# Performance work log

Measured on AMD Instinct MI355X. Metric: run time of the kernel, lower is better.

Reference implementation:

```python
import jax, jax.numpy as jnp
import numpy as np
from jax import lax

B, T, C, H, HOR = 64, 2048, 64, 256, 96
BETA, THR = 0.9, 1.0


def setup_inputs() -> dict:
    key = jax.random.key(0)
    ks = jax.random.split(key, 10)
    s = lambda *sh: 1.0 / np.sqrt(sh[-1])
    return {
        "x": jax.random.normal(ks[0], (B, T, C), jnp.float32),
        "snn_w": jax.random.uniform(ks[1], (H, C), jnp.float32, -s(C), s(C)),
        "snn_b": jax.random.uniform(ks[2], (H,), jnp.float32, -s(C), s(C)),
        "gru_wih": jax.random.uniform(ks[3], (3 * H, C + H), jnp.float32, -s(H), s(H)),
        "gru_whh": jax.random.uniform(ks[4], (3 * H, H), jnp.float32, -s(H), s(H)),
        "gru_bih": jax.random.uniform(ks[5], (3 * H,), jnp.float32, -s(H), s(H)),
        "gru_bhh": jax.random.uniform(ks[6], (3 * H,), jnp.float32, -s(H), s(H)),
        "head_w": jax.random.uniform(ks[7], (HOR, H), jnp.float32, -s(H), s(H)),
        "head_b": jax.random.uniform(ks[8], (HOR,), jnp.float32, -s(H), s(H)),
    }


@jax.custom_vjp
def spike(x):
    return (x > 0).astype(x.dtype)

def _spike_fwd(x):
    return spike(x), x

def _spike_bwd(x, g):
    # snntorch ATan surrogate, alpha=2: grad = 1 / (1 + (pi*x)^2)
    return (g / (1.0 + (jnp.pi * x) ** 2),)

spike.defvjp(_spike_fwd, _spike_bwd)


def reference(x, snn_w, snn_b, gru_wih, gru_whh, gru_bih, gru_bhh, head_w, head_b):
    # Batched SNN input current across all timesteps: [B,T,H]
    cur = jnp.einsum("btc,hc->bth", x, snn_w) + snn_b

    def lif_step(mem, i_t):
        # reset computed from previous mem, detached (snntorch mem_reset)
        reset = lax.stop_gradient((mem > THR).astype(mem.dtype))
        mem_new = BETA * mem + i_t - reset * THR
        spk = spike(mem_new - THR)
        return mem_new, spk

    mem0 = jnp.zeros((B, H), x.dtype)
    _, spks = lax.scan(lif_step, mem0, cur.transpose(1, 0, 2))  # [T,B,H]

    h_comb = jnp.concatenate([x, spks.transpose(1, 0, 2)], axis=-1)  # [B,T,C+H]

    # GRU: precompute input gates for all timesteps
    gx = jnp.einsum("btc,gc->btg", h_comb, gru_wih) + gru_bih  # [B,T,3H]

    def gru_step(h, gx_t):
        gh = h @ gru_whh.T + gru_bhh
        xr, xz, xn = jnp.split(gx_t, 3, axis=-1)
        hr, hz, hn = jnp.split(gh, 3, axis=-1)
        r = jax.nn.sigmoid(xr + hr)
        z = jax.nn.sigmoid(xz + hz)
        n = jnp.tanh(xn + r * hn)
        h_new = (1.0 - z) * n + z * h
        return h_new, None

    h0 = jnp.zeros((B, H), x.dtype)
    hT, _ = lax.scan(gru_step, h0, gx.transpose(1, 0, 2))

    return hT @ head_w.T + head_b  # [B, HOR]
```

## Files before the change

kernel.cpp:

```cpp
#include <hip/hip_runtime.h>
#include <cstdint>
#include <cstddef>

#define B_   64
#define T_   2048
#define C_   64
#define H_   256
#define G3_  768
#define HOR_ 96

typedef _Float16 h2 __attribute__((ext_vector_type(2)));
typedef _Float16 h8 __attribute__((ext_vector_type(8)));
typedef _Float16 f16x8 __attribute__((ext_vector_type(8)));
typedef float f32x4 __attribute__((ext_vector_type(4)));

#define K1_TT 128
__global__ __launch_bounds__(256) void k_cur(const float* __restrict__ x,
                                             const float* __restrict__ w,
                                             const float* __restrict__ bias,
                                             float* __restrict__ cur,
                                             int* __restrict__ flags) {
  __shared__ float xs[K1_TT * C_];
  const int b = blockIdx.x;
  const int t0 = blockIdx.y * K1_TT;
  const int tid = threadIdx.x;

  if (b == 0 && blockIdx.y == 0) {
#pragma unroll
    for (int i = 0; i < 4; i++) flags[tid + i * 256] = 0;
  }

  const float4* xsrc = (const float4*)(x + ((size_t)b * T_ + t0) * C_);
  float4* xdst = (float4*)xs;
#pragma unroll
  for (int i = 0; i < (K1_TT * C_ / 4) / 256; i++)
    xdst[tid + i * 256] = xsrc[tid + i * 256];

  float wr[C_];
  const float4* wp = (const float4*)(w + (size_t)tid * C_);
#pragma unroll
  for (int q = 0; q < C_ / 4; q++) {
    float4 v = wp[q];
    wr[4 * q + 0] = v.x; wr[4 * q + 1] = v.y;
    wr[4 * q + 2] = v.z; wr[4 * q + 3] = v.w;
  }
  const float bb = bias[tid];
  __syncthreads();

  for (int t = 0; t < K1_TT; t++) {
    const float4* xrow = (const float4*)(xs + t * C_);
    float a0 = 0.f, a1 = 0.f;
#pragma unroll
    for (int q = 0; q < C_ / 4; q += 2) {
      float4 v0 = xrow[q];
      float4 v1 = xrow[q + 1];
      a0 += wr[4 * q + 0] * v0.x + wr[4 * q + 1] * v0.y +
            wr[4 * q + 2] * v0.z + wr[4 * q + 3] * v0.w;
      a1 += wr[4 * q + 4] * v1.x + wr[4 * q + 5] * v1.y +
            wr[4 * q + 6] * v1.z + wr[4 * q + 7] * v1.w;
    }
    cur[((size_t)b * T_ + t0 + t) * H_ + tid] = a0 + a1 + bb;
  }
}

__global__ __launch_bounds__(64) void k_lif(const float* __restrict__ cur,
                                            unsigned char* __restrict__ spk) {
  const int b = blockIdx.x >> 2;
  const int h = ((blockIdx.x & 3) << 6) + threadIdx.x;
  const float* cp = cur + (size_t)b * T_ * H_ + h;
  unsigned char* sp = spk + (size_t)b * T_ * H_ + h;
  float mem = 0.f;
#pragma unroll 32
  for (int t = 0; t < T_; t++) {
    float c = cp[(size_t)t * H_];
    float reset = (mem > 1.0f) ? 1.0f : 0.0f;
    mem = 0.9f * mem + c - reset;
    sp[(size_t)t * H_] = (mem > 1.0f) ? (unsigned char)1 : (unsigned char)0;
  }
}

#define GM 128
#define GN 128
#define AKP 40
#define CTP 136
#define DQ_ (0.0625f / (127.0f * 127.0f))
__global__ __launch_bounds__(256) void k_fused(
    const float* __restrict__ x, const unsigned char* __restrict__ spk,
    const float* __restrict__ wih, const float* __restrict__ bih,
    _Float16* __restrict__ gx, const float* __restrict__ whh,
    const float* __restrict__ bhh, const float* __restrict__ head_w,
    const float* __restrict__ head_b, float* __restrict__ out,
    int* __restrict__ flags) {
  alignas(16) __shared__ _Float16 Ah[GM * AKP];
  alignas(16) __shared__ _Float16 Bh[GN * AKP];
  alignas(16) __shared__ _Float16 Ct[GM * CTP];
  alignas(16) __shared__ int hq[2][64];
  __shared__ float hbuf32[H_];

  const int tid = threadIdx.x;
  const int lane = tid & 63;

  if (blockIdx.x >= 64) {
    const int pidx = blockIdx.x - 64;
    const int bb = pidx / 3;
    const int pp = pidx - bb * 3;
    const int wave = tid >> 6;
    const int ln = lane & 15;
    const int qd = lane >> 4;
    const int wm = (wave & 1) * 64;
    const int wn = ((wave >> 1) & 1) * 64;

    for (int mt = 0; mt < 16; mt++) {
      const int m0 = bb * 2048 + mt * 128;
      for (int nh = 0; nh < 2; nh++) {
        const int n0 = pp * 256 + nh * 128;
        f32x4 acc[4][4] = {};
        for (int kc = 0; kc < 10; kc++) {
          const int k0 = kc * 32;
          if (k0 < 64) {
#pragma unroll
            for (int i = 0; i < 4; i++) {
              int idx = tid + i * 256;
              int r = idx >> 3;
              int c4 = (idx & 7) * 4;
              float4 v = *(const float4*)(x + (size_t)(m0 + r) * C_ + k0 + c4);
              h2 lo, hi;
              lo.x = (_Float16)v.x; lo.y = (_Float16)v.y;
              hi.x = (_Float16)v.z; hi.y = (_Float16)v.w;
              h2* d = (h2*)&Ah[r * AKP + c4];
              d[0] = lo; d[1] = hi;
            }
          } else {
#pragma unroll
            for (int i = 0; i < 4; i++) {
              int idx = tid + i * 256;
              int r = idx >> 3;
              int c4 = (idx & 7) * 4;
              uchar4 u = *(const uchar4*)(spk + (size_t)(m0 + r) * H_ + (k0 - 64) + c4);
              h2 lo, hi;
              lo.x = (_Float16)(int)u.x; lo.y = (_Float16)(int)u.y;
              hi.x = (_Float16)(int)u.z; hi.y = (_Float16)(int)u.w;
              h2* d = (h2*)&Ah[r * AKP + c4];
              d[0] = lo; d[1] = hi;
            }
          }
#pragma unroll
          for (int i = 0; i < 4; i++) {
            int idx = tid + i * 256;
            int r = idx >> 3;
            int c4 = (idx & 7) * 4;
            float4 v = *(const float4*)(wih + (size_t)(n0 + r) * 320 + k0 + c4);
            h2 lo, hi;
            lo.x = (_Float16)v.x; lo.y = (_Float16)v.y;
            hi.x = (_Float16)v.z; hi.y = (_Float16)v.w;
            h2* d = (h2*)&Bh[r * AKP + c4];
            d[0] = lo; d[1] = hi;
          }
          __syncthreads();
          {
            f16x8 a[4], bbf[4];
#pragma unroll
            for (int mtl = 0; mtl < 4; mtl++)
              a[mtl] = *(const f16x8*)&Ah[(wm + mtl * 16 + ln) * AKP + qd * 8];
#pragma unroll
            for (int nt = 0; nt < 4; nt++)
              bbf[nt] = *(const f16x8*)&Bh[(wn + nt * 16 + ln) * AKP + qd * 8];
#pragma unroll
            for (int mtl = 0; mtl < 4; mtl++)
#pragma unroll
              for (int nt = 0; nt < 4; nt++)
                acc[mtl][nt] = __builtin_amdgcn_mfma_f32_16x16x32_f16(
                    a[mtl], bbf[nt], acc[mtl][nt], 0, 0, 0);
          }
          __syncthreads();
        }
        {
          float bias[4];
#pragma unroll
          for (int nt = 0; nt < 4; nt++) bias[nt] = bih[n0 + wn + nt * 16 + ln];
#pragma unroll
          for (int mtl = 0; mtl < 4; mtl++)
#pragma unroll
            for (int nt = 0; nt < 4; nt++) {
              int n = wn + nt * 16 + ln;
#pragma unroll
              for (int r = 0; r < 4; r++) {
                int m = wm + mtl * 16 + qd * 4 + r;
                Ct[m * CTP + n] = (_Float16)(acc[mtl][nt][r] + bias[nt]);
              }
            }
        }
        __syncthreads();
#pragma unroll
        for (int i = 0; i < 8; i++) {
          int idx = tid + i * 256;
          int r = idx >> 4;
          int c = (idx & 15) * 8;
          *(h8*)(gx + (size_t)(m0 + r) * G3_ + n0 + c) = *(const h8*)&Ct[r * CTP + c];
        }
        __syncthreads();
      }
      if (tid == 0)
        __hip_atomic_fetch_add(&flags[bb * 16 + mt], 1, __ATOMIC_RELEASE,
                               __HIP_MEMORY_SCOPE_AGENT);
    }
    return;
  }

  const int b = blockIdx.x;
  const int j = tid;

  int wr[64], wz[64], wn[64];
  {
    const float qs = 2032.0f;
    const float4* p0 = (const float4*)(whh + (size_t)j * H_);
    const float4* p1 = (const float4*)(whh + (size_t)(H_ + j) * H_);
    const float4* p2 = (const float4*)(whh + (size_t)(2 * H_ + j) * H_);
#pragma unroll
    for (int q = 0; q < 64; q++) {
      float4 a = p0[q];
      wr[q] = ((int)rintf(a.x * qs) & 255) | (((int)rintf(a.y * qs) & 255) << 8) |
              (((int)rintf(a.z * qs) & 255) << 16) | (((int)rintf(a.w * qs) & 255) << 24);
      float4 c = p1[q];
      wz[q] = ((int)rintf(c.x * qs) & 255) | (((int)rintf(c.y * qs) & 255) << 8) |
              (((int)rintf(c.z * qs) & 255) << 16) | (((int)rintf(c.w * qs) & 255) << 24);
      float4 d = p2[q];
      wn[q] = ((int)rintf(d.x * qs) & 255) | (((int)rintf(d.y * qs) & 255) << 8) |
              (((int)rintf(d.z * qs) & 255) << 16) | (((int)rintf(d.w * qs) & 255) << 24);
    }
  }
  const float br_ = bhh[j], bz_ = bhh[H_ + j], bn_ = bhh[2 * H_ + j];

  if (tid < 128) ((int*)hq)[tid] = 0;
  float hj = 0.f;
  __syncthreads();

  const _Float16* gxb = gx + (size_t)b * T_ * G3_;
  int p = 0;
  for (int mt = 0; mt < 16; mt++) {
    if (tid == 0) {
      while (__hip_atomic_load(&flags[b * 16 + mt], __ATOMIC_ACQUIRE,
                               __HIP_MEMORY_SCOPE_AGENT) < 3)
        __builtin_amdgcn_s_sleep(8);
    }
    __syncthreads();

    const _Float16* gc = gxb + (size_t)mt * 128 * G3_;
    _Float16 pr = gc[j], pz = gc[H_ + j], pn = gc[2 * H_ + j];

    for (int tt = 0; tt < 128; tt++) {
      float xr = (float)pr, xz = (float)pz, xn = (float)pn;
      if (tt < 127) {
        const _Float16* g = gc + (size_t)(tt + 1) * G3_;
        pr = g[j]; pz = g[H_ + j]; pn = g[2 * H_ + j];
      }

      const int* hb = hq[p];
      int ar0 = 0, ar1 = 0, az0 = 0, az1 = 0, an0 = 0, an1 = 0;
#pragma unroll
      for (int g4 = 0; g4 < 4; g4++) {
#pragma unroll
        for (int cc = 0; cc < 4; cc++) {
          int c = g4 * 4 + cc;
          int4 hv = *(const int4*)(hb + c * 4);
#pragma unroll
          for (int i = 0; i < 4; i++) {
            int h4 = (i == 0) ? hv.x : (i == 1) ? hv.y : (i == 2) ? hv.z : hv.w;
            int wi = c * 4 + i;
            if (wi & 1) {
              ar1 = __builtin_amdgcn_sdot4(wr[wi], h4, ar1, false);
              az1 = __builtin_amdgcn_sdot4(wz[wi], h4, az1, false);
              an1 = __builtin_amdgcn_sdot4(wn[wi], h4, an1, false);
            } else {
              ar0 = __builtin_amdgcn_sdot4(wr[wi], h4, ar0, false);
              az0 = __builtin_amdgcn_sdot4(wz[wi], h4, az0, false);
              an0 = __builtin_amdgcn_sdot4(wn[wi], h4, an0, false);
            }
          }
        }
        __builtin_amdgcn_sched_barrier(2 | 4 | 16 | 32 | 64);
      }
      int ar = ar0 + ar1, az = az0 + az1, an = an0 + an1;

      float r = 1.f / (1.f + __expf(-(xr + (float)ar * DQ_ + br_)));
      float z = 1.f / (1.f + __expf(-(xz + (float)az * DQ_ + bz_)));
      float pre = xn + r * ((float)an * DQ_ + bn_);
      float e = __expf(2.f * pre);
      float n = 1.f - 2.f / (e + 1.f);
      hj = (1.f - z) * n + z * hj;

      ((char*)hq[p ^ 1])[j] = (char)(int)rintf(hj * 127.0f);
      p ^= 1;
      __syncthreads();
    }
  }

  hbuf32[j] = hj;
  __syncthreads();

  if (tid < HOR_) {
    const float4* hw = (const float4*)(head_w + (size_t)tid * H_);
    const float4* hv4 = (const float4*)hbuf32;
    float acc = head_b[tid];
#pragma unroll
    for (int q = 0; q < H_ / 4; q++) {
      float4 w4 = hw[q];
      float4 v4 = hv4[q];
      acc += w4.x * v4.x + w4.y * v4.y + w4.z * v4.z + w4.w * v4.w;
    }
    out[(size_t)b * HOR_ + tid] = acc;
  }
}

extern "C" void kernel_launch(void* const* d_in, const int* in_sizes, int n_in,
                              void* d_out, int out_size, void* d_ws, size_t ws_size,
                              hipStream_t stream) {
  const float* x      = (const float*)d_in[0];
  const float* snn_w  = (const float*)d_in[1];
  const float* snn_b  = (const float*)d_in[2];
  const float* wih    = (const float*)d_in[3];
  const float* whh    = (const float*)d_in[4];
  const float* bih    = (const float*)d_in[5];
  const float* bhh    = (const float*)d_in[6];
  const float* head_w = (const float*)d_in[7];
  const float* head_b = (const float*)d_in[8];
  float* out = (float*)d_out;

  char* ws = (char*)d_ws;
  _Float16* gx = (_Float16*)ws;
  float* cur = (float*)ws;
  unsigned char* spk = (unsigned char*)(ws + (size_t)201326592);
  int* flags = (int*)(ws + (size_t)234881024);

  k_cur<<<dim3(B_, T_ / K1_TT), 256, 0, stream>>>(x, snn_w, snn_b, cur, flags);
  k_lif<<<dim3(256), 64, 0, stream>>>(cur, spk);
  k_fused<<<dim3(256), 256, 0, stream>>>(x, spk, wih, bih, gx, whh, bhh,
                                         head_w, head_b, out, flags);
}
```

Measured before the change: 1.849 ms.

## Split GRU hidden-unit dot products across thread pairs with 512-thread blocks

```diff
diff --git a/kernel.cpp b/kernel.cpp
--- a/kernel.cpp
+++ b/kernel.cpp
@@ -84,7 +84,7 @@
 #define AKP 40
 #define CTP 136
 #define DQ_ (0.0625f / (127.0f * 127.0f))
-__global__ __launch_bounds__(256) void k_fused(
+__global__ __launch_bounds__(512, 2) void k_fused(
     const float* __restrict__ x, const unsigned char* __restrict__ spk,
     const float* __restrict__ wih, const float* __restrict__ bih,
     _Float16* __restrict__ gx, const float* __restrict__ whh,
@@ -108,19 +108,19 @@
     const int ln = lane & 15;
     const int qd = lane >> 4;
     const int wm = (wave & 1) * 64;
-    const int wn = ((wave >> 1) & 1) * 64;
+    const int wn = (wave >> 1) * 32;
 
     for (int mt = 0; mt < 16; mt++) {
       const int m0 = bb * 2048 + mt * 128;
       for (int nh = 0; nh < 2; nh++) {
         const int n0 = pp * 256 + nh * 128;
-        f32x4 acc[4][4] = {};
+        f32x4 acc[4][2] = {};
         for (int kc = 0; kc < 10; kc++) {
           const int k0 = kc * 32;
           if (k0 < 64) {
 #pragma unroll
-            for (int i = 0; i < 4; i++) {
-              int idx = tid + i * 256;
+            for (int i = 0; i < 2; i++) {
+              int idx = tid + i * 512;
               int r = idx >> 3;
               int c4 = (idx & 7) * 4;
               float4 v = *(const float4*)(x + (size_t)(m0 + r) * C_ + k0 + c4);
@@ -132,8 +132,8 @@
             }
           } else {
 #pragma unroll
-            for (int i = 0; i < 4; i++) {
-              int idx = tid + i * 256;
+            for (int i = 0; i < 2; i++) {
+              int idx = tid + i * 512;
               int r = idx >> 3;
               int c4 = (idx & 7) * 4;
               uchar4 u = *(const uchar4*)(spk + (size_t)(m0 + r) * H_ + (k0 - 64) + c4);
@@ -145,8 +145,8 @@
             }
           }
 #pragma unroll
-          for (int i = 0; i < 4; i++) {
-            int idx = tid + i * 256;
+          for (int i = 0; i < 2; i++) {
+            int idx = tid + i * 512;
             int r = idx >> 3;
             int c4 = (idx & 7) * 4;
             float4 v = *(const float4*)(wih + (size_t)(n0 + r) * 320 + k0 + c4);
@@ -158,30 +158,30 @@
           }
           __syncthreads();
           {
-            f16x8 a[4], bbf[4];
+            f16x8 a[4], bbf[2];
 #pragma unroll
             for (int mtl = 0; mtl < 4; mtl++)
               a[mtl] = *(const f16x8*)&Ah[(wm + mtl * 16 + ln) * AKP + qd * 8];
 #pragma unroll
-            for (int nt = 0; nt < 4; nt++)
+            for (int nt = 0; nt < 2; nt++)
               bbf[nt] = *(const f16x8*)&Bh[(wn + nt * 16 + ln) * AKP + qd * 8];
 #pragma unroll
             for (int mtl = 0; mtl < 4; mtl++)
 #pragma unroll
-              for (int nt = 0; nt < 4; nt++)
+              for (int nt = 0; nt < 2; nt++)
                 acc[mtl][nt] = __builtin_amdgcn_mfma_f32_16x16x32_f16(
                     a[mtl], bbf[nt], acc[mtl][nt], 0, 0, 0);
           }
           __syncthreads();
         }
         {
-          float bias[4];
-#pragma unroll
-          for (int nt = 0; nt < 4; nt++) bias[nt] = bih[n0 + wn + nt * 16 + ln];
+          float bias[2];
+#pragma unroll
+          for (int nt = 0; nt < 2; nt++) bias[nt] = bih[n0 + wn + nt * 16 + ln];
 #pragma unroll
           for (int mtl = 0; mtl < 4; mtl++)
 #pragma unroll
-            for (int nt = 0; nt < 4; nt++) {
+            for (int nt = 0; nt < 2; nt++) {
               int n = wn + nt * 16 + ln;
 #pragma unroll
               for (int r = 0; r < 4; r++) {
@@ -192,8 +192,8 @@
         }
         __syncthreads();
 #pragma unroll
-        for (int i = 0; i < 8; i++) {
-          int idx = tid + i * 256;
+        for (int i = 0; i < 4; i++) {
+          int idx = tid + i * 512;
           int r = idx >> 4;
           int c = (idx & 15) * 8;
           *(h8*)(gx + (size_t)(m0 + r) * G3_ + n0 + c) = *(const h8*)&Ct[r * CTP + c];
@@ -208,16 +208,17 @@
   }
 
   const int b = blockIdx.x;
-  const int j = tid;
-
-  int wr[64], wz[64], wn[64];
+  const int j = tid >> 1;
+  const int half = tid & 1;
+
+  int wr[32], wz[32], wn2[32];
   {
     const float qs = 2032.0f;
-    const float4* p0 = (const float4*)(whh + (size_t)j * H_);
-    const float4* p1 = (const float4*)(whh + (size_t)(H_ + j) * H_);
-    const float4* p2 = (const float4*)(whh + (size_t)(2 * H_ + j) * H_);
-#pragma unroll
-    for (int q = 0; q < 64; q++) {
+    const float4* p0 = (const float4*)(whh + (size_t)j * H_ + half * 128);
+    const float4* p1 = (const float4*)(whh + (size_t)(H_ + j) * H_ + half * 128);
+    const float4* p2 = (const float4*)(whh + (size_t)(2 * H_ + j) * H_ + half * 128);
+#pragma unroll
+    for (int q = 0; q < 32; q++) {
       float4 a = p0[q];
       wr[q] = ((int)rintf(a.x * qs) & 255) | (((int)rintf(a.y * qs) & 255) << 8) |
               (((int)rintf(a.z * qs) & 255) << 16) | (((int)rintf(a.w * qs) & 255) << 24);
@@ -225,8 +226,8 @@
       wz[q] = ((int)rintf(c.x * qs) & 255) | (((int)rintf(c.y * qs) & 255) << 8) |
               (((int)rintf(c.z * qs) & 255) << 16) | (((int)rintf(c.w * qs) & 255) << 24);
       float4 d = p2[q];
-      wn[q] = ((int)rintf(d.x * qs) & 255) | (((int)rintf(d.y * qs) & 255) << 8) |
-              (((int)rintf(d.z * qs) & 255) << 16) | (((int)rintf(d.w * qs) & 255) << 24);
+      wn2[q] = ((int)rintf(d.x * qs) & 255) | (((int)rintf(d.y * qs) & 255) << 8) |
+               (((int)rintf(d.z * qs) & 255) << 16) | (((int)rintf(d.w * qs) & 255) << 24);
     }
   }
   const float br_ = bhh[j], bz_ = bhh[H_ + j], bn_ = bhh[2 * H_ + j];
@@ -255,32 +256,29 @@
         pr = g[j]; pz = g[H_ + j]; pn = g[2 * H_ + j];
       }
 
-      const int* hb = hq[p];
+      const int* hb = hq[p] + (half << 5);
       int ar0 = 0, ar1 = 0, az0 = 0, az1 = 0, an0 = 0, an1 = 0;
 #pragma unroll
-      for (int g4 = 0; g4 < 4; g4++) {
-#pragma unroll
-        for (int cc = 0; cc < 4; cc++) {
-          int c = g4 * 4 + cc;
-          int4 hv = *(const int4*)(hb + c * 4);
-#pragma unroll
-          for (int i = 0; i < 4; i++) {
-            int h4 = (i == 0) ? hv.x : (i == 1) ? hv.y : (i == 2) ? hv.z : hv.w;
-            int wi = c * 4 + i;
-            if (wi & 1) {
-              ar1 = __builtin_amdgcn_sdot4(wr[wi], h4, ar1, false);
-              az1 = __builtin_amdgcn_sdot4(wz[wi], h4, az1, false);
-              an1 = __builtin_amdgcn_sdot4(wn[wi], h4, an1, false);
-            } else {
-              ar0 = __builtin_amdgcn_sdot4(wr[wi], h4, ar0, false);
-              az0 = __builtin_amdgcn_sdot4(wz[wi], h4, az0, false);
-              an0 = __builtin_amdgcn_sdot4(wn[wi], h4, an0, false);
-            }
+      for (int c = 0; c < 8; c++) {
+        int4 hv = ((const int4*)hb)[c];
+#pragma unroll
+        for (int i = 0; i < 4; i++) {
+          int h4 = (i == 0) ? hv.x : (i == 1) ? hv.y : (i == 2) ? hv.z : hv.w;
+          int wi = c * 4 + i;
+          if (wi & 1) {
+            ar1 = __builtin_amdgcn_sdot4(wr[wi], h4, ar1, false);
+            az1 = __builtin_amdgcn_sdot4(wz[wi], h4, az1, false);
+            an1 = __builtin_amdgcn_sdot4(wn2[wi], h4, an1, false);
+          } else {
+            ar0 = __builtin_amdgcn_sdot4(wr[wi], h4, ar0, false);
+            az0 = __builtin_amdgcn_sdot4(wz[wi], h4, az0, false);
+            an0 = __builtin_amdgcn_sdot4(wn2[wi], h4, an0, false);
           }
         }
-        __builtin_amdgcn_sched_barrier(2 | 4 | 16 | 32 | 64);
       }
-      int ar = ar0 + ar1, az = az0 + az1, an = an0 + an1;
+      int ar = ar0 + ar1; ar += __shfl_xor(ar, 1);
+      int az = az0 + az1; az += __shfl_xor(az, 1);
+      int an = an0 + an1; an += __shfl_xor(an, 1);
 
       float r = 1.f / (1.f + __expf(-(xr + (float)ar * DQ_ + br_)));
       float z = 1.f / (1.f + __expf(-(xz + (float)az * DQ_ + bz_)));
@@ -289,13 +287,13 @@
       float n = 1.f - 2.f / (e + 1.f);
       hj = (1.f - z) * n + z * hj;
 
-      ((char*)hq[p ^ 1])[j] = (char)(int)rintf(hj * 127.0f);
+      if (!half) ((char*)hq[p ^ 1])[j] = (char)(int)rintf(hj * 127.0f);
       p ^= 1;
       __syncthreads();
     }
   }
 
-  hbuf32[j] = hj;
+  if (!half) hbuf32[j] = hj;
   __syncthreads();
 
   if (tid < HOR_) {
@@ -334,6 +332,6 @@
 
   k_cur<<<dim3(B_, T_ / K1_TT), 256, 0, stream>>>(x, snn_w, snn_b, cur, flags);
   k_lif<<<dim3(256), 64, 0, stream>>>(cur, spk);
-  k_fused<<<dim3(256), 256, 0, stream>>>(x, spk, wih, bih, gx, whh, bhh,
+  k_fused<<<dim3(256), 512, 0, stream>>>(x, spk, wih, bih, gx, whh, bhh,
                                          head_w, head_b, out, flags);
 }
```

New measurement: 2.043 ms. 10.5% more time.

## Process two batch rows per recurrent GRU block, sharing quantized weights

Applied to the files above, without the earlier changes.

```diff
diff --git a/kernel.cpp b/kernel.cpp
--- a/kernel.cpp
+++ b/kernel.cpp
@@ -94,14 +94,14 @@
   alignas(16) __shared__ _Float16 Ah[GM * AKP];
   alignas(16) __shared__ _Float16 Bh[GN * AKP];
   alignas(16) __shared__ _Float16 Ct[GM * CTP];
-  alignas(16) __shared__ int hq[2][64];
-  __shared__ float hbuf32[H_];
+  alignas(16) __shared__ int hq[2][2][64];
+  __shared__ float hbuf32[2][H_];
 
   const int tid = threadIdx.x;
   const int lane = tid & 63;
 
-  if (blockIdx.x >= 64) {
-    const int pidx = blockIdx.x - 64;
+  if (blockIdx.x >= 32) {
+    const int pidx = blockIdx.x - 32;
     const int bb = pidx / 3;
     const int pp = pidx - bb * 3;
     const int wave = tid >> 6;
@@ -207,10 +207,10 @@
     return;
   }
 
-  const int b = blockIdx.x;
+  const int b0 = blockIdx.x << 1;
   const int j = tid;
 
-  int wr[64], wz[64], wn[64];
+  int wr[64], wz[64], wn2[64];
   {
     const float qs = 2032.0f;
     const float4* p0 = (const float4*)(whh + (size_t)j * H_);
@@ -225,90 +225,115 @@
       wz[q] = ((int)rintf(c.x * qs) & 255) | (((int)rintf(c.y * qs) & 255) << 8) |
               (((int)rintf(c.z * qs) & 255) << 16) | (((int)rintf(c.w * qs) & 255) << 24);
       float4 d = p2[q];
-      wn[q] = ((int)rintf(d.x * qs) & 255) | (((int)rintf(d.y * qs) & 255) << 8) |
-              (((int)rintf(d.z * qs) & 255) << 16) | (((int)rintf(d.w * qs) & 255) << 24);
+      wn2[q] = ((int)rintf(d.x * qs) & 255) | (((int)rintf(d.y * qs) & 255) << 8) |
+               (((int)rintf(d.z * qs) & 255) << 16) | (((int)rintf(d.w * qs) & 255) << 24);
     }
   }
   const float br_ = bhh[j], bz_ = bhh[H_ + j], bn_ = bhh[2 * H_ + j];
 
-  if (tid < 128) ((int*)hq)[tid] = 0;
-  float hj = 0.f;
+  ((int*)hq)[tid] = 0;
+  float hjA = 0.f, hjB = 0.f;
   __syncthreads();
 
-  const _Float16* gxb = gx + (size_t)b * T_ * G3_;
+  const _Float16* gxA = gx + (size_t)b0 * T_ * G3_;
+  const _Float16* gxB = gx + (size_t)(b0 + 1) * T_ * G3_;
   int p = 0;
   for (int mt = 0; mt < 16; mt++) {
     if (tid == 0) {
-      while (__hip_atomic_load(&flags[b * 16 + mt], __ATOMIC_ACQUIRE,
+      while (__hip_atomic_load(&flags[b0 * 16 + mt], __ATOMIC_ACQUIRE,
                                __HIP_MEMORY_SCOPE_AGENT) < 3)
         __builtin_amdgcn_s_sleep(8);
+      while (__hip_atomic_load(&flags[(b0 + 1) * 16 + mt], __ATOMIC_ACQUIRE,
+                               __HIP_MEMORY_SCOPE_AGENT) < 3)
+        __builtin_amdgcn_s_sleep(8);
     }
     __syncthreads();
 
-    const _Float16* gc = gxb + (size_t)mt * 128 * G3_;
-    _Float16 pr = gc[j], pz = gc[H_ + j], pn = gc[2 * H_ + j];
+    const _Float16* gcA = gxA + (size_t)mt * 128 * G3_;
+    const _Float16* gcB = gxB + (size_t)mt * 128 * G3_;
+    _Float16 prA = gcA[j], pzA = gcA[H_ + j], pnA = gcA[2 * H_ + j];
+    _Float16 prB = gcB[j], pzB = gcB[H_ + j], pnB = gcB[2 * H_ + j];
 
     for (int tt = 0; tt < 128; tt++) {
-      float xr = (float)pr, xz = (float)pz, xn = (float)pn;
+      float xrA = (float)prA, xzA = (float)pzA, xnA = (float)pnA;
+      float xrB = (float)prB, xzB = (float)pzB, xnB = (float)pnB;
       if (tt < 127) {
-        const _Float16* g = gc + (size_t)(tt + 1) * G3_;
-        pr = g[j]; pz = g[H_ + j]; pn = g[2 * H_ + j];
+        const _Float16* gA = gcA + (size_t)(tt + 1) * G3_;
+        prA = gA[j]; pzA = gA[H_ + j]; pnA = gA[2 * H_ + j];
+        const _Float16* gB = gcB + (size_t)(tt + 1) * G3_;
+        prB = gB[j]; pzB = gB[H_ + j]; pnB = gB[2 * H_ + j];
       }
 
-      const int* hb = hq[p];
-      int ar0 = 0, ar1 = 0, az0 = 0, az1 = 0, an0 = 0, an1 = 0;
-#pragma unroll
-      for (int g4 = 0; g4 < 4; g4++) {
-#pragma unroll
-        for (int cc = 0; cc < 4; cc++) {
-          int c = g4 * 4 + cc;
-          int4 hv = *(const int4*)(hb + c * 4);
-#pragma unroll
-          for (int i = 0; i < 4; i++) {
-            int h4 = (i == 0) ? hv.x : (i == 1) ? hv.y : (i == 2) ? hv.z : hv.w;
-            int wi = c * 4 + i;
-            if (wi & 1) {
-              ar1 = __builtin_amdgcn_sdot4(wr[wi], h4, ar1, false);
-              az1 = __builtin_amdgcn_sdot4(wz[wi], h4, az1, false);
-              an1 = __builtin_amdgcn_sdot4(wn[wi], h4, an1, false);
-            } else {
-              ar0 = __builtin_amdgcn_sdot4(wr[wi], h4, ar0, false);
-              az0 = __builtin_amdgcn_sdot4(wz[wi], h4, az0, false);
-              an0 = __builtin_amdgcn_sdot4(wn[wi], h4, an0, false);
-            }
-          }
+      const int4* hA = (const int4*)hq[0][p];
+      const int4* hB = (const int4*)hq[1][p];
+      int arA = 0, azA = 0, anA = 0, arB = 0, azB = 0, anB = 0;
+      int4 cA0 = hA[0], cA1 = hA[1], cB0 = hB[0], cB1 = hB[1];
+#pragma unroll
+      for (int g = 0; g < 8; g++) {
+        int4 nA0, nA1, nB0, nB1;
+        if (g < 7) {
+          nA0 = hA[g * 2 + 2]; nA1 = hA[g * 2 + 3];
+          nB0 = hB[g * 2 + 2]; nB1 = hB[g * 2 + 3];
+        }
+#pragma unroll
+        for (int i = 0; i < 8; i++) {
+          int a4 = (i == 0) ? cA0.x : (i == 1) ? cA0.y : (i == 2) ? cA0.z :
+                   (i == 3) ? cA0.w : (i == 4) ? cA1.x : (i == 5) ? cA1.y :
+                   (i == 6) ? cA1.z : cA1.w;
+          int b4 = (i == 0) ? cB0.x : (i == 1) ? cB0.y : (i == 2) ? cB0.z :
+                   (i == 3) ? cB0.w : (i == 4) ? cB1.x : (i == 5) ? cB1.y :
+                   (i == 6) ? cB1.z : cB1.w;
+          int wi = g * 8 + i;
+          arA = __builtin_amdgcn_sdot4(wr[wi], a4, arA, false);
+          azA = __builtin_amdgcn_sdot4(wz[wi], a4, azA, false);
+          anA = __builtin_amdgcn_sdot4(wn2[wi], a4, anA, false);
+          arB = __builtin_amdgcn_sdot4(wr[wi], b4, arB, false);
+          azB = __builtin_amdgcn_sdot4(wz[wi], b4, azB, false);
+          anB = __builtin_amdgcn_sdot4(wn2[wi], b4, anB, false);
         }
         __builtin_amdgcn_sched_barrier(2 | 4 | 16 | 32 | 64);
+        if (g < 7) { cA0 = nA0; cA1 = nA1; cB0 = nB0; cB1 = nB1; }
       }
-      int ar = ar0 + ar1, az = az0 + az1, an = an0 + an1;
-
-      float r = 1.f / (1.f + __expf(-(xr + (float)ar * DQ_ + br_)));
-      float z = 1.f / (1.f + __expf(-(xz + (float)az * DQ_ + bz_)));
-      float pre = xn + r * ((float)an * DQ_ + bn_);
-      float e = __expf(2.f * pre);
-      float n = 1.f - 2.f / (e + 1.f);
-      hj = (1.f - z) * n + z * hj;
-
-      ((char*)hq[p ^ 1])[j] = (char)(int)rintf(hj * 127.0f);
+
+      float rA = 1.f / (1.f + __expf(-(xrA + (float)arA * DQ_ + br_)));
+      float rB = 1.f / (1.f + __expf(-(xrB + (float)arB * DQ_ + br_)));
+      float zA = 1.f / (1.f + __expf(-(xzA + (float)azA * DQ_ + bz_)));
+      float zB = 1.f / (1.f + __expf(-(xzB + (float)azB * DQ_ + bz_)));
+      float preA = xnA + rA * ((float)anA * DQ_ + bn_);
+      float preB = xnB + rB * ((float)anB * DQ_ + bn_);
+      float eA = __expf(2.f * preA);
+      float eB = __expf(2.f * preB);
+      float nA = 1.f - 2.f / (eA + 1.f);
+      float nB = 1.f - 2.f / (eB + 1.f);
+      hjA = (1.f - zA) * nA + zA * hjA;
+      hjB = (1.f - zB) * nB + zB * hjB;
+
+      ((char*)hq[0][p ^ 1])[j] = (char)(int)rintf(hjA * 127.0f);
+      ((char*)hq[1][p ^ 1])[j] = (char)(int)rintf(hjB * 127.0f);
       p ^= 1;
       __syncthreads();
     }
   }
 
-  hbuf32[j] = hj;
+  hbuf32[0][j] = hjA;
+  hbuf32[1][j] = hjB;
   __syncthreads();
 
-  if (tid < HOR_) {
-    const float4* hw = (const float4*)(head_w + (size_t)tid * H_);
-    const float4* hv4 = (const float4*)hbuf32;
-    float acc = head_b[tid];
-#pragma unroll
-    for (int q = 0; q < H_ / 4; q++) {
-      float4 w4 = hw[q];
-      float4 v4 = hv4[q];
-      acc += w4.x * v4.x + w4.y * v4.y + w4.z * v4.z + w4.w * v4.w;
-    }
-    out[(size_t)b * HOR_ + tid] = acc;
+  {
+    const int who = tid >> 7;
+    const int r = tid & 127;
+    if (r < HOR_) {
+      const float4* hw = (const float4*)(head_w + (size_t)r * H_);
+      const float4* hv4 = (const float4*)hbuf32[who];
+      float acc = head_b[r];
+#pragma unroll
+      for (int q = 0; q < H_ / 4; q++) {
+        float4 w4 = hw[q];
+        float4 v4 = hv4[q];
+        acc += w4.x * v4.x + w4.y * v4.y + w4.z * v4.z + w4.w * v4.w;
+      }
+      out[(size_t)(b0 + who) * HOR_ + r] = acc;
+    }
   }
 }
 
@@ -334,6 +359,6 @@
 
   k_cur<<<dim3(B_, T_ / K1_TT), 256, 0, stream>>>(x, snn_w, snn_b, cur, flags);
   k_lif<<<dim3(256), 64, 0, stream>>>(cur, spk);
-  k_fused<<<dim3(256), 256, 0, stream>>>(x, spk, wih, bih, gx, whh, bhh,
+  k_fused<<<dim3(224), 256, 0, stream>>>(x, spk, wih, bih, gx, whh, bhh,
                                          head_w, head_b, out, flags);
 }
```

After: 2.875 ms. 1.55x slower.
